# Performance work log

Hardware: AMD Instinct MI355X
Metric: run time of the kernel (lower is better)

The kernel has to match this reference:

```python
import jax, jax.numpy as jnp
import numpy as np

EPS = 1e-5


def _conv(x, w, padding, groups=1):
    return jax.lax.conv_general_dilated(
        x, w, window_strides=(1, 1),
        padding=[(padding, padding), (padding, padding)],
        dimension_numbers=("NCHW", "OIHW", "NCHW"),
        feature_group_count=groups)


def _bn(x, gamma, beta, mean, var):
    # inference-mode BatchNorm2d, params shape [C]
    inv = gamma * jax.lax.rsqrt(var + EPS)
    return x * inv[None, :, None, None] + (beta - mean * inv)[None, :, None, None]


def _adder_dw(x, w):
    # depthwise AdderNet 'conv': out[b, c*R+r, h, w] = -sum_{kh,kw} |x[b,c,h+kh-p,w+kw-p] - w[c,r,kh,kw]|
    # x: [B,C,H,W], w: [C,R,K,K] (groups=C, R outputs per group)
    B, C, H, W = x.shape
    R, K = w.shape[1], w.shape[-1]
    p = K // 2
    xp = jnp.pad(x, ((0, 0), (0, 0), (p, p), (p, p)))
    acc = jnp.zeros((B, C, R, H, W), x.dtype)
    for kh in range(K):          # fixed small 3x3 tap loop
        for kw in range(K):
            shift = xp[:, :, kh:kh + H, kw:kw + W]          # [B,C,H,W]
            tap = w[:, :, kh, kw]                           # [C,R]
            acc = acc + jnp.abs(shift[:, :, None] - tap[None, :, :, None, None])
    return -acc.reshape(B, C * R, H, W)


def setup_inputs() -> dict:
    key = jax.random.key(0)
    ks = jax.random.split(key, 12)
    B, Cin, H, W = 32, 240, 56, 56
    init_c, ratio = 24, 10
    r1 = ratio - 1            # 9 ghost channels per primary channel
    new_c = init_c * r1       # 216
    f32 = jnp.float32
    x = jax.random.normal(ks[0], (B, Cin, H, W), f32)
    w_primary = jax.random.normal(ks[1], (init_c, Cin, 1, 1), f32) * 0.05
    w_dw = jax.random.normal(ks[2], (init_c, 1, 3, 3), f32) * 0.1
    w_add = jax.random.normal(ks[3], (init_c, r1, 3, 3), f32) * 0.1
    def bn(kk, c):
        k1, k2 = jax.random.split(kk)
        return (jnp.ones((c,), f32), jnp.zeros((c,), f32),
                jax.random.normal(k1, (c,), f32) * 0.1,
                jax.random.uniform(k2, (c,), f32, 0.5, 1.5))
    g1, b1, m1, v1 = bn(ks[4], init_c)
    g2, b2, m2, v2 = bn(ks[5], init_c)
    g3, b3, m3, v3 = bn(ks[6], new_c)
    return dict(x=x, w_primary=w_primary, g1=g1, b1=b1, m1=m1, v1=v1,
                w_dw=w_dw, g2=g2, b2=b2, m2=m2, v2=v2,
                w_add=w_add, g3=g3, b3=b3, m3=m3, v3=v3)


def reference(x, w_primary, g1, b1, m1, v1, w_dw, g2, b2, m2, v2,
              w_add, g3, b3, m3, v3):
    oup = 240
    init_c = w_primary.shape[0]
    # primary_conv: 1x1 conv -> BN -> depthwise 3x3 conv -> BN -> Identity (relu slot is Identity)
    x1 = _conv(x, w_primary, padding=0)
    x1 = _bn(x1, g1, b1, m1, v1)
    x1 = _conv(x1, w_dw, padding=1, groups=init_c)
    x1 = _bn(x1, g2, b2, m2, v2)
    # cheap_operation: depthwise Adder2D -> BN -> ReLU
    x2 = _adder_dw(x1, w_add)
    x2 = jax.nn.relu(_bn(x2, g3, b3, m3, v3))
    out = jnp.concatenate([x1, x2], axis=1)
    return out[:, :oup]
```

## Files before the change

### kernel.cpp

```cpp
#include <hip/hip_runtime.h>

#define EPS_ 1e-5f
#define BATCH 32
#define CIN 240
#define H_ 56
#define W_ 56
#define HW 3136
#define C1 24
#define R_ 9
#define C2 216
#define COUT 240

#define WS_WT   0
#define WS_B1   5760
#define WS_WDW  5784
#define WS_B2   6000
#define WS_INV3 6024
#define WS_T3   6240

__global__ __launch_bounds__(256) void prep_kernel(
    const float* __restrict__ wp,
    const float* __restrict__ g1, const float* __restrict__ b1,
    const float* __restrict__ m1, const float* __restrict__ v1,
    const float* __restrict__ wdw,
    const float* __restrict__ g2, const float* __restrict__ b2,
    const float* __restrict__ m2, const float* __restrict__ v2,
    const float* __restrict__ g3, const float* __restrict__ b3,
    const float* __restrict__ m3, const float* __restrict__ v3,
    float* __restrict__ ws) {
  int i = blockIdx.x * 256 + threadIdx.x;
  if (i < 5760) {
    int ci = i / C1, co = i % C1;
    float s = g1[co] / sqrtf(v1[co] + EPS_);
    ws[WS_WT + ci * C1 + co] = wp[co * CIN + ci] * s;
    if (ci == 0) ws[WS_B1 + co] = b1[co] - m1[co] * s;
  } else if (i < 5760 + C2) {
    int j = i - 5760;
    int c = j / 9;
    float s = g2[c] / sqrtf(v2[c] + EPS_);
    ws[WS_WDW + j] = wdw[j] * s;
    if (j % 9 == 0) ws[WS_B2 + c] = b2[c] - m2[c] * s;
  } else if (i < 5976 + C2) {
    int j = i - 5976;
    float s = g3[j] / sqrtf(v3[j] + EPS_);
    ws[WS_INV3 + j] = s;
    ws[WS_T3 + j] = b3[j] - m3[j] * s;
  }
}

__global__ __launch_bounds__(256) void conv1x1_kernel(
    const float* __restrict__ x, const float* __restrict__ wt,
    const float* __restrict__ bias1, float* __restrict__ out) {
  int p  = blockIdx.x * 256 + threadIdx.x;
  int b  = p / HW;
  int hw = p - b * HW;
  const float* xb = x + (size_t)b * CIN * HW + hw;

  float acc[C1];
#pragma unroll
  for (int co = 0; co < C1; ++co) acc[co] = 0.f;

#pragma unroll 8
  for (int ci = 0; ci < CIN; ++ci) {
    float xv = xb[(size_t)ci * HW];
    const float* wr = wt + ci * C1;
#pragma unroll
    for (int co = 0; co < C1; ++co) acc[co] = fmaf(wr[co], xv, acc[co]);
  }

  float* o = out + ((size_t)b * COUT + C1) * HW + hw;
#pragma unroll
  for (int co = 0; co < C1; ++co) o[(size_t)co * HW] = acc[co] + bias1[co];
}

__global__ __launch_bounds__(256) void dw_kernel(
    const float* __restrict__ outr, const float* __restrict__ wdwf,
    const float* __restrict__ bias2, float* __restrict__ out) {
  int p = blockIdx.x * 256 + threadIdx.x;
  if (p >= HW) return;
  int c = blockIdx.y, b = blockIdx.z;
  int h = p / W_, w = p - h * W_;
  const float* in = outr + ((size_t)b * COUT + C1 + c) * HW;
  const float* wk = wdwf + c * 9;
  float acc = bias2[c];
#pragma unroll
  for (int kh = 0; kh < 3; ++kh) {
    int hh = h + kh - 1;
    if (hh < 0 || hh >= H_) continue;
#pragma unroll
    for (int kw = 0; kw < 3; ++kw) {
      int ww = w + kw - 1;
      if (ww < 0 || ww >= W_) continue;
      acc = fmaf(in[hh * W_ + ww], wk[kh * 3 + kw], acc);
    }
  }
  out[((size_t)b * COUT + c) * HW + p] = acc;
}

__global__ __launch_bounds__(256) void adder_kernel(
    const float* __restrict__ outr, const float* __restrict__ wadd,
    const float* __restrict__ inv3, const float* __restrict__ t3,
    float* __restrict__ out) {
  int p = blockIdx.x * 256 + threadIdx.x;
  if (p >= HW) return;
  int c = blockIdx.y, b = blockIdx.z;
  int h = p / W_, w = p - h * W_;
  const float* in = outr + ((size_t)b * COUT + c) * HW;

  float xv[9];
#pragma unroll
  for (int kh = 0; kh < 3; ++kh) {
#pragma unroll
    for (int kw = 0; kw < 3; ++kw) {
      int hh = h + kh - 1, ww = w + kw - 1;
      bool ok = (hh >= 0) & (hh < H_) & (ww >= 0) & (ww < W_);
      xv[kh * 3 + kw] = ok ? in[hh * W_ + ww] : 0.f;
    }
  }

#pragma unroll
  for (int r = 0; r < R_; ++r) {
    int j = c * R_ + r;
    const float* tp = wadd + j * 9;
    float acc = 0.f;
#pragma unroll
    for (int k = 0; k < 9; ++k) acc += fabsf(xv[k] - tp[k]);
    float y = fmaf(-inv3[j], acc, t3[j]);
    out[((size_t)b * COUT + (C1 + j)) * HW + p] = fmaxf(y, 0.f);
  }
}

extern "C" void kernel_launch(void* const* d_in, const int* in_sizes, int n_in,
                              void* d_out, int out_size, void* d_ws, size_t ws_size,
                              hipStream_t stream) {
  const float* x    = (const float*)d_in[0];
  const float* wp   = (const float*)d_in[1];
  const float* g1   = (const float*)d_in[2];
  const float* b1   = (const float*)d_in[3];
  const float* m1   = (const float*)d_in[4];
  const float* v1   = (const float*)d_in[5];
  const float* wdw  = (const float*)d_in[6];
  const float* g2   = (const float*)d_in[7];
  const float* b2   = (const float*)d_in[8];
  const float* m2   = (const float*)d_in[9];
  const float* v2   = (const float*)d_in[10];
  const float* wadd = (const float*)d_in[11];
  const float* g3   = (const float*)d_in[12];
  const float* b3   = (const float*)d_in[13];
  const float* m3   = (const float*)d_in[14];
  const float* v3   = (const float*)d_in[15];

  float* ws  = (float*)d_ws;
  float* out = (float*)d_out;

  prep_kernel<<<25, 256, 0, stream>>>(wp, g1, b1, m1, v1, wdw, g2, b2, m2, v2,
                                      g3, b3, m3, v3, ws);

  conv1x1_kernel<<<392, 256, 0, stream>>>(x, ws + WS_WT, ws + WS_B1, out);

  dw_kernel<<<dim3(13, C1, BATCH), 256, 0, stream>>>(out, ws + WS_WDW,
                                                     ws + WS_B2, out);

  adder_kernel<<<dim3(13, C1, BATCH), 256, 0, stream>>>(out, wadd, ws + WS_INV3,
                                                        ws + WS_T3, out);
}
```

Before: 230.4 us.

## Restructure conv1x1 with split-K waves and smem weights; vectorize adder kernel

The 1x1 conv now stages the folded weights in shared memory. Each thread computes 4 pixels by 24 channels with float4 loads, and the 240 input channels are split across 4 waves, whose partial sums are then reduced through shared memory. The adder kernel handles 4 adjacent pixels per thread, uses float4 row loads, keeps taps and BN params in shared memory, and writes with float4 stores, so the grid shrinks to 4 x-blocks. This targets memory-access efficiency and weight reload cost, in exchange for high register pressure (96 accumulators) and extra shared-memory reduction syncs.

New measurement: 245.4 us. 6.5% more time.

```diff
diff --git a/kernel.cpp b/kernel.cpp
--- a/kernel.cpp
+++ b/kernel.cpp
@@ -51,26 +51,89 @@
 __global__ __launch_bounds__(256) void conv1x1_kernel(
     const float* __restrict__ x, const float* __restrict__ wt,
     const float* __restrict__ bias1, float* __restrict__ out) {
-  int p  = blockIdx.x * 256 + threadIdx.x;
-  int b  = p / HW;
-  int hw = p - b * HW;
-  const float* xb = x + (size_t)b * CIN * HW + hw;
-
-  float acc[C1];
-#pragma unroll
-  for (int co = 0; co < C1; ++co) acc[co] = 0.f;
-
-#pragma unroll 8
-  for (int ci = 0; ci < CIN; ++ci) {
-    float xv = xb[(size_t)ci * HW];
-    const float* wr = wt + ci * C1;
-#pragma unroll
-    for (int co = 0; co < C1; ++co) acc[co] = fmaf(wr[co], xv, acc[co]);
-  }
-
-  float* o = out + ((size_t)b * COUT + C1) * HW + hw;
-#pragma unroll
-  for (int co = 0; co < C1; ++co) o[(size_t)co * HW] = acc[co] + bias1[co];
+  __shared__ float smem[12288];
+  const int tid  = threadIdx.x;
+  const int lane = tid & 63;
+  const int wv   = tid >> 6;
+
+  for (int i = tid; i < 5760; i += 256) smem[i] = wt[i];
+  __syncthreads();
+
+  const int P  = blockIdx.x * 256 + lane * 4;
+  const int b  = P / HW;
+  const int hw = P - b * HW;
+  const float* xp = x + (size_t)(b * CIN) * HW + hw;
+
+  float acc[96];
+#pragma unroll
+  for (int i = 0; i < 96; ++i) acc[i] = 0.f;
+
+  const int ci0 = wv * 60;
+#pragma unroll 4
+  for (int ci = 0; ci < 60; ++ci) {
+    const float4 xv = *(const float4*)(xp + (size_t)(ci0 + ci) * HW);
+    const float* wr = &smem[(ci0 + ci) * C1];
+#pragma unroll
+    for (int k = 0; k < 6; ++k) {
+      const float4 wq = *(const float4*)(wr + 4 * k);
+      const int o = 16 * k;
+      acc[o+ 0] = fmaf(wq.x, xv.x, acc[o+ 0]);
+      acc[o+ 1] = fmaf(wq.x, xv.y, acc[o+ 1]);
+      acc[o+ 2] = fmaf(wq.x, xv.z, acc[o+ 2]);
+      acc[o+ 3] = fmaf(wq.x, xv.w, acc[o+ 3]);
+      acc[o+ 4] = fmaf(wq.y, xv.x, acc[o+ 4]);
+      acc[o+ 5] = fmaf(wq.y, xv.y, acc[o+ 5]);
+      acc[o+ 6] = fmaf(wq.y, xv.z, acc[o+ 6]);
+      acc[o+ 7] = fmaf(wq.y, xv.w, acc[o+ 7]);
+      acc[o+ 8] = fmaf(wq.z, xv.x, acc[o+ 8]);
+      acc[o+ 9] = fmaf(wq.z, xv.y, acc[o+ 9]);
+      acc[o+10] = fmaf(wq.z, xv.z, acc[o+10]);
+      acc[o+11] = fmaf(wq.z, xv.w, acc[o+11]);
+      acc[o+12] = fmaf(wq.w, xv.x, acc[o+12]);
+      acc[o+13] = fmaf(wq.w, xv.y, acc[o+13]);
+      acc[o+14] = fmaf(wq.w, xv.z, acc[o+14]);
+      acc[o+15] = fmaf(wq.w, xv.w, acc[o+15]);
+    }
+  }
+  __syncthreads();
+
+  float* red0 = smem;
+  float* red1 = smem + 6144;
+
+  if (wv == 2) {
+#pragma unroll
+    for (int i = 0; i < 96; ++i) red0[i * 64 + lane] = acc[i];
+  } else if (wv == 3) {
+#pragma unroll
+    for (int i = 0; i < 96; ++i) red1[i * 64 + lane] = acc[i];
+  }
+  __syncthreads();
+  if (wv == 0) {
+#pragma unroll
+    for (int i = 0; i < 96; ++i) acc[i] += red0[i * 64 + lane];
+  } else if (wv == 1) {
+#pragma unroll
+    for (int i = 0; i < 96; ++i) acc[i] += red1[i * 64 + lane];
+  }
+  __syncthreads();
+  if (wv == 1) {
+#pragma unroll
+    for (int i = 0; i < 96; ++i) red0[i * 64 + lane] = acc[i];
+  }
+  __syncthreads();
+  if (wv == 0) {
+    float* o = out + ((size_t)b * COUT + C1) * HW + hw;
+#pragma unroll
+    for (int co = 0; co < C1; ++co) {
+      const float bb = bias1[co];
+      float4 v;
+      v.x = acc[co*4+0] + red0[(co*4+0)*64 + lane] + bb;
+      v.y = acc[co*4+1] + red0[(co*4+1)*64 + lane] + bb;
+      v.z = acc[co*4+2] + red0[(co*4+2)*64 + lane] + bb;
+      v.w = acc[co*4+3] + red0[(co*4+3)*64 + lane] + bb;
+      *(float4*)(o + (size_t)co * HW) = v;
+    }
+  }
 }
 
 __global__ __launch_bounds__(256) void dw_kernel(
@@ -101,32 +164,63 @@
     const float* __restrict__ outr, const float* __restrict__ wadd,
     const float* __restrict__ inv3, const float* __restrict__ t3,
     float* __restrict__ out) {
-  int p = blockIdx.x * 256 + threadIdx.x;
-  if (p >= HW) return;
-  int c = blockIdx.y, b = blockIdx.z;
-  int h = p / W_, w = p - h * W_;
+  const int c = blockIdx.y, b = blockIdx.z;
+  __shared__ float taps[R_][3][4];
+  __shared__ float s3[R_], t3s[R_];
+  const int tid = threadIdx.x;
+  if (tid < 108) {
+    int r = tid / 12, kh = (tid / 4) % 3, kw = tid & 3;
+    taps[r][kh][kw] = (kw < 3) ? wadd[((c * R_ + r) * 3 + kh) * 3 + kw] : 0.f;
+  } else if (tid >= 128 && tid < 128 + R_) {
+    int r = tid - 128;
+    s3[r]  = inv3[c * R_ + r];
+    t3s[r] = t3[c * R_ + r];
+  }
+  __syncthreads();
+
+  const int q = blockIdx.x * 256 + tid;
+  if (q >= 784) return;
+  const int h  = q / 14;
+  const int w0 = (q - h * 14) * 4;
   const float* in = outr + ((size_t)b * COUT + c) * HW;
 
-  float xv[9];
+  float xr[3][6];
 #pragma unroll
   for (int kh = 0; kh < 3; ++kh) {
-#pragma unroll
-    for (int kw = 0; kw < 3; ++kw) {
-      int hh = h + kh - 1, ww = w + kw - 1;
-      bool ok = (hh >= 0) & (hh < H_) & (ww >= 0) & (ww < W_);
-      xv[kh * 3 + kw] = ok ? in[hh * W_ + ww] : 0.f;
-    }
+    const int hh = h + kh - 1;
+    const bool rok = (hh >= 0) & (hh < H_);
+    const float* rp = in + hh * W_;
+    xr[kh][0] = (rok && w0 > 0) ? rp[w0 - 1] : 0.f;
+    if (rok) {
+      const float4 m = *(const float4*)(rp + w0);
+      xr[kh][1] = m.x; xr[kh][2] = m.y; xr[kh][3] = m.z; xr[kh][4] = m.w;
+    } else {
+      xr[kh][1] = 0.f; xr[kh][2] = 0.f; xr[kh][3] = 0.f; xr[kh][4] = 0.f;
+    }
+    xr[kh][5] = (rok && w0 < W_ - 4) ? rp[w0 + 4] : 0.f;
   }
 
 #pragma unroll
   for (int r = 0; r < R_; ++r) {
-    int j = c * R_ + r;
-    const float* tp = wadd + j * 9;
-    float acc = 0.f;
-#pragma unroll
-    for (int k = 0; k < 9; ++k) acc += fabsf(xv[k] - tp[k]);
-    float y = fmaf(-inv3[j], acc, t3[j]);
-    out[((size_t)b * COUT + (C1 + j)) * HW + p] = fmaxf(y, 0.f);
+    float a0 = 0.f, a1 = 0.f, a2 = 0.f, a3 = 0.f;
+#pragma unroll
+    for (int kh = 0; kh < 3; ++kh) {
+#pragma unroll
+      for (int kw = 0; kw < 3; ++kw) {
+        const float t = taps[r][kh][kw];
+        a0 += fabsf(xr[kh][kw + 0] - t);
+        a1 += fabsf(xr[kh][kw + 1] - t);
+        a2 += fabsf(xr[kh][kw + 2] - t);
+        a3 += fabsf(xr[kh][kw + 3] - t);
+      }
+    }
+    const float s = s3[r], bb = t3s[r];
+    float4 v;
+    v.x = fmaxf(fmaf(-s, a0, bb), 0.f);
+    v.y = fmaxf(fmaf(-s, a1, bb), 0.f);
+    v.z = fmaxf(fmaf(-s, a2, bb), 0.f);
+    v.w = fmaxf(fmaf(-s, a3, bb), 0.f);
+    *(float4*)(out + ((size_t)b * COUT + C1 + c * R_ + r) * HW + h * W_ + w0) = v;
   }
 }
 
@@ -161,6 +255,6 @@
   dw_kernel<<<dim3(13, C1, BATCH), 256, 0, stream>>>(out, ws + WS_WDW,
                                                      ws + WS_B2, out);
 
-  adder_kernel<<<dim3(13, C1, BATCH), 256, 0, stream>>>(out, wadd, ws + WS_INV3,
-                                                        ws + WS_T3, out);
-}
+  adder_kernel<<<dim3(4, C1, BATCH), 256, 0, stream>>>(out, wadd, ws + WS_INV3,
+                                                       ws + WS_T3, out);
+}
```
